# Performance work log

Hardware: AMD Instinct MI355X
Metric: run time of the kernel (lower is better)

The kernel has to match this reference:

```python
import jax, jax.numpy as jnp
import numpy as np

DIM = 4096
N_HEADS = 32
HEAD_DIM = 128
N_KV_HEADS = 8
REPEAT = N_HEADS // N_KV_HEADS  # 4
B = 8
# ragged per-sequence lengths, fixed so total token count is static (jit-friendly)
SEQLEN = np.array([1024, 3072, 2048, 2560, 1536, 2048, 1792, 2304], dtype=np.int64)
TOTAL = int(SEQLEN.sum())  # 16384


def setup_inputs() -> dict:
    key = jax.random.key(0)
    k1, k2, k3 = jax.random.split(key, 3)
    embedding = jax.random.normal(k1, (B, DIM), dtype=jnp.float32)
    # nn.Linear weights: stored as [out_features, in_features]
    W_up = jax.random.normal(k2, (N_KV_HEADS * HEAD_DIM, DIM), dtype=jnp.float32) * (DIM ** -0.5)
    W_down = jax.random.normal(k3, (DIM, N_HEADS * HEAD_DIM), dtype=jnp.float32) * ((N_HEADS * HEAD_DIM) ** -0.5)
    seqlen = jnp.asarray(SEQLEN)
    return {"embedding": embedding, "W_up": W_up, "W_down": W_down, "seqlen": seqlen}


def reference(embedding, W_up, W_down, seqlen):
    # up-projection: [B, dim] -> [B, n_kv_heads*head_dim]
    x = embedding @ W_up.T
    # split kv heads and repeat-interleave to n_heads: [B, n_kv, hd] -> [B, n_heads, hd]
    xv = x.reshape(B, N_KV_HEADS, HEAD_DIM)
    val = jnp.repeat(xv, REPEAT, axis=1).reshape(B, N_HEADS * HEAD_DIM)  # [B, dim]
    # ragged broadcast: row i repeated seqlen[i] times -> [TOTAL, dim]
    out = jnp.repeat(val, seqlen, axis=0, total_repeat_length=TOTAL)
    # down-projection on every token row (redundant per-sequence math, as in original)
    return out @ W_down.T  # [TOTAL, dim]
```

## Files before the change

### kernel.cpp

```cpp
#include <hip/hip_runtime.h>

#define DIM   4096
#define KVDIM 1024
#define NB    8
#define TOTAL 16384
#define BCAST_BLOCKS 4096

__global__ __launch_bounds__(256)
void k_up(const float* __restrict__ emb, const float* __restrict__ wup,
          float* __restrict__ x) {
    int wid  = blockIdx.x * 4 + (threadIdx.x >> 6);
    int lane = threadIdx.x & 63;
    int j = wid >> 3;
    int b = wid & 7;
    const float4* e = (const float4*)(emb + b * DIM);
    const float4* w = (const float4*)(wup + (long)j * DIM);
    float acc = 0.f;
    #pragma unroll
    for (int ii = 0; ii < DIM / 4 / 64; ii++) {
        int it = ii * 64 + lane;
        float4 ev = e[it], wv = w[it];
        acc += ev.x * wv.x + ev.y * wv.y + ev.z * wv.z + ev.w * wv.w;
    }
    #pragma unroll
    for (int off = 32; off; off >>= 1) acc += __shfl_down(acc, off, 64);
    if (lane == 0) x[b * KVDIM + j] = acc;
}

__global__ __launch_bounds__(256)
void k_down(const float* __restrict__ x, const float* __restrict__ wdn,
            float* __restrict__ y) {
    __shared__ float part[4][NB];
    int o    = blockIdx.x;
    int wv   = threadIdx.x >> 6;
    int lane = threadIdx.x & 63;
    const float4* w = (const float4*)(wdn + (long)o * DIM);
    float acc[NB];
    #pragma unroll
    for (int b = 0; b < NB; b++) acc[b] = 0.f;
    #pragma unroll
    for (int ii = 0; ii < 4; ii++) {
        int it = wv * 256 + ii * 64 + lane;
        int k0 = it * 4;
        int kv = ((k0 >> 9) << 7) + (k0 & 127);
        float4 wvv = w[it];
        #pragma unroll
        for (int b = 0; b < NB; b++) {
            const float4 xv = *(const float4*)(x + b * KVDIM + kv);
            acc[b] += xv.x * wvv.x + xv.y * wvv.y + xv.z * wvv.z + xv.w * wvv.w;
        }
    }
    #pragma unroll
    for (int b = 0; b < NB; b++) {
        #pragma unroll
        for (int off = 32; off; off >>= 1) acc[b] += __shfl_down(acc[b], off, 64);
    }
    if (lane == 0) {
        #pragma unroll
        for (int b = 0; b < NB; b++) part[wv][b] = acc[b];
    }
    __syncthreads();
    if (threadIdx.x < NB) {
        int b = threadIdx.x;
        float s = part[0][b] + part[1][b] + part[2][b] + part[3][b];
        y[b * DIM + o] = s;
    }
}

__global__ __launch_bounds__(256)
void k_bcast(const float* __restrict__ y, const int* __restrict__ seqlen,
             float4* __restrict__ out) {
    int c0 = seqlen[0];
    int c1 = c0 + seqlen[1];
    int c2 = c1 + seqlen[2];
    int c3 = c2 + seqlen[3];
    int c4 = c3 + seqlen[4];
    int c5 = c4 + seqlen[5];
    int c6 = c5 + seqlen[6];
    #pragma unroll
    for (int g = 0; g < TOTAL / BCAST_BLOCKS; g++) {
        int row = blockIdx.x + g * BCAST_BLOCKS;
        int s = (row >= c0) + (row >= c1) + (row >= c2) + (row >= c3)
              + (row >= c4) + (row >= c5) + (row >= c6);
        const float4* yr = (const float4*)(y + s * DIM);
        float4* orow = out + (long)row * (DIM / 4);
        #pragma unroll
        for (int c = threadIdx.x; c < DIM / 4; c += 256)
            orow[c] = yr[c];
    }
}

extern "C" void kernel_launch(void* const* d_in, const int* in_sizes, int n_in,
                              void* d_out, int out_size, void* d_ws, size_t ws_size,
                              hipStream_t stream) {
    const float* emb = (const float*)d_in[0];
    const float* wup = (const float*)d_in[1];
    const float* wdn = (const float*)d_in[2];
    const int* seqlen = (const int*)d_in[3];

    float* x = (float*)d_ws;
    float* y = x + NB * KVDIM;

    k_up   <<<NB * KVDIM / 4, 256, 0, stream>>>(emb, wup, x);
    k_down <<<DIM,            256, 0, stream>>>(x, wdn, y);
    k_bcast<<<BCAST_BLOCKS,   256, 0, stream>>>(y, seqlen, (float4*)d_out);
}
```

Before: 348.0 us.

## Fuse up-proj, down-proj and broadcast into one cooperative kernel with grid syncs

Replaces the three separate launches with a single cooperative kernel of 1024 blocks that runs the up-projection, a grid-wide sync, the down-projection (one wave per output column), another grid sync, and the ragged row broadcast. The aim is to remove two launch gaps and the kernel-boundary drain between stages. In exchange it uses a smaller grid for the bandwidth-bound broadcast and adds grid-barrier cost. It falls back to the old three-kernel path if the cooperative launch fails.

Measured after the change: 519.2 us. 49.2% more time.

```diff
diff --git a/kernel.cpp b/kernel.cpp
--- a/kernel.cpp
+++ b/kernel.cpp
@@ -1,10 +1,86 @@
 #include <hip/hip_runtime.h>
+#include <hip/hip_cooperative_groups.h>
+
+namespace cg = cooperative_groups;
 
 #define DIM   4096
 #define KVDIM 1024
 #define NB    8
 #define TOTAL 16384
+#define NBLK  1024
 #define BCAST_BLOCKS 4096
+
+__global__ __launch_bounds__(256, 4)
+void fused_pca(const float* __restrict__ emb, const float* __restrict__ wup,
+               const float* __restrict__ wdn, const int* __restrict__ seqlen,
+               float* __restrict__ x, float* __restrict__ y,
+               float* __restrict__ out) {
+    cg::grid_group grid = cg::this_grid();
+    const int lane = threadIdx.x & 63;
+    const int wid  = blockIdx.x * 4 + (threadIdx.x >> 6);
+
+    #pragma unroll
+    for (int i = 0; i < 2; i++) {
+        int d = wid * 2 + i;
+        int j = d >> 3;
+        int b = d & 7;
+        const float4* e = (const float4*)(emb + b * DIM);
+        const float4* w = (const float4*)(wup + (long)j * DIM);
+        float acc = 0.f;
+        for (int it = lane; it < DIM / 4; it += 64) {
+            float4 ev = e[it], wv = w[it];
+            acc += ev.x * wv.x + ev.y * wv.y + ev.z * wv.z + ev.w * wv.w;
+        }
+        #pragma unroll
+        for (int off = 32; off; off >>= 1) acc += __shfl_down(acc, off, 64);
+        if (lane == 0) x[b * KVDIM + j] = acc;
+    }
+
+    grid.sync();
+
+    {
+        int o = wid;
+        const float4* w = (const float4*)(wdn + (long)o * DIM);
+        float acc[NB];
+        #pragma unroll
+        for (int b = 0; b < NB; b++) acc[b] = 0.f;
+        for (int it = lane; it < DIM / 4; it += 64) {
+            int k0 = it * 4;
+            int kv = ((k0 >> 9) << 7) + (k0 & 127);
+            float4 wv = w[it];
+            #pragma unroll
+            for (int b = 0; b < NB; b++) {
+                const float4 xv = *(const float4*)(x + b * KVDIM + kv);
+                acc[b] += xv.x * wv.x + xv.y * wv.y + xv.z * wv.z + xv.w * wv.w;
+            }
+        }
+        #pragma unroll
+        for (int b = 0; b < NB; b++) {
+            #pragma unroll
+            for (int off = 32; off; off >>= 1) acc[b] += __shfl_down(acc[b], off, 64);
+            if (lane == 0) y[b * DIM + o] = acc[b];
+        }
+    }
+
+    grid.sync();
+
+    int c0 = seqlen[0];
+    int c1 = c0 + seqlen[1];
+    int c2 = c1 + seqlen[2];
+    int c3 = c2 + seqlen[3];
+    int c4 = c3 + seqlen[4];
+    int c5 = c4 + seqlen[5];
+    int c6 = c5 + seqlen[6];
+    for (int g = 0; g < TOTAL / NBLK; g++) {
+        int row = blockIdx.x + g * NBLK;
+        int s = (row >= c0) + (row >= c1) + (row >= c2) + (row >= c3)
+              + (row >= c4) + (row >= c5) + (row >= c6);
+        const float4* yr = (const float4*)(y + s * DIM);
+        float4* orow = (float4*)(out + (long)row * DIM);
+        for (int c = threadIdx.x; c < DIM / 4; c += 256)
+            orow[c] = yr[c];
+    }
+}
 
 __global__ __launch_bounds__(256)
 void k_up(const float* __restrict__ emb, const float* __restrict__ wup,
@@ -62,8 +138,7 @@
     __syncthreads();
     if (threadIdx.x < NB) {
         int b = threadIdx.x;
-        float s = part[0][b] + part[1][b] + part[2][b] + part[3][b];
-        y[b * DIM + o] = s;
+        y[b * DIM + o] = part[0][b] + part[1][b] + part[2][b] + part[3][b];
     }
 }
 
@@ -100,8 +175,16 @@
 
     float* x = (float*)d_ws;
     float* y = x + NB * KVDIM;
+    float* out = (float*)d_out;
 
-    k_up   <<<NB * KVDIM / 4, 256, 0, stream>>>(emb, wup, x);
-    k_down <<<DIM,            256, 0, stream>>>(x, wdn, y);
-    k_bcast<<<BCAST_BLOCKS,   256, 0, stream>>>(y, seqlen, (float4*)d_out);
+    void* args[] = {(void*)&emb, (void*)&wup, (void*)&wdn, (void*)&seqlen,
+                    (void*)&x, (void*)&y, (void*)&out};
+    hipError_t err = hipLaunchCooperativeKernel((const void*)fused_pca,
+                                                dim3(NBLK), dim3(256),
+                                                args, 0, stream);
+    if (err != hipSuccess) {
+        k_up   <<<NB * KVDIM / 4, 256, 0, stream>>>(emb, wup, x);
+        k_down <<<DIM,            256, 0, stream>>>(x, wdn, y);
+        k_bcast<<<BCAST_BLOCKS,   256, 0, stream>>>(y, seqlen, (float4*)out);
+    }
 }
```

## Fuse down-projection and broadcast with per-column-tile atomic counters

Applied to the files above, without the earlier changes.

Merges the down-projection and ragged broadcast kernels into one 1024-block kernel. Each block computes four output columns, then signals a per-64-column-tile counter. Blocks spin-wait until their tile's counter is complete and then write 64-column slabs of the output, so broadcast writes can start before the whole down-projection finishes. This removes one launch and the gap between kernels. It relies on all 64 producer blocks for a tile being co-resident or scheduled ahead, so it carries deadlock risk, and the output write pattern changes to 256-byte row segments.

Result: slower. 645.4 us (+85.5%).

```diff
diff --git a/kernel.cpp b/kernel.cpp
--- a/kernel.cpp
+++ b/kernel.cpp
@@ -4,11 +4,12 @@
 #define KVDIM 1024
 #define NB    8
 #define TOTAL 16384
-#define BCAST_BLOCKS 4096
+#define GRID2 1024
 
 __global__ __launch_bounds__(256)
 void k_up(const float* __restrict__ emb, const float* __restrict__ wup,
-          float* __restrict__ x) {
+          float* __restrict__ x, int* __restrict__ cnt) {
+    if (blockIdx.x == 0 && threadIdx.x < 16) cnt[threadIdx.x] = 0;
     int wid  = blockIdx.x * 4 + (threadIdx.x >> 6);
     int lane = threadIdx.x & 63;
     int j = wid >> 3;
@@ -17,7 +18,7 @@
     const float4* w = (const float4*)(wup + (long)j * DIM);
     float acc = 0.f;
     #pragma unroll
-    for (int ii = 0; ii < DIM / 4 / 64; ii++) {
+    for (int ii = 0; ii < 16; ii++) {
         int it = ii * 64 + lane;
         float4 ev = e[it], wv = w[it];
         acc += ev.x * wv.x + ev.y * wv.y + ev.z * wv.z + ev.w * wv.w;
@@ -28,65 +29,96 @@
 }
 
 __global__ __launch_bounds__(256)
-void k_down(const float* __restrict__ x, const float* __restrict__ wdn,
-            float* __restrict__ y) {
-    __shared__ float part[4][NB];
-    int o    = blockIdx.x;
-    int wv   = threadIdx.x >> 6;
-    int lane = threadIdx.x & 63;
-    const float4* w = (const float4*)(wdn + (long)o * DIM);
-    float acc[NB];
+void k_dc(const float* __restrict__ x, const float* __restrict__ wdn,
+          float* __restrict__ y, int* __restrict__ cnt,
+          const int* __restrict__ seqlen, float4* __restrict__ out) {
+    __shared__ float4 tile[NB][65];
+    __shared__ float  part[4][NB];
+    const int B    = blockIdx.x;
+    const int t    = threadIdx.x;
+    const int wv   = t >> 6;
+    const int lane = t & 63;
+
     #pragma unroll
-    for (int b = 0; b < NB; b++) acc[b] = 0.f;
-    #pragma unroll
-    for (int ii = 0; ii < 4; ii++) {
-        int it = wv * 256 + ii * 64 + lane;
-        int k0 = it * 4;
-        int kv = ((k0 >> 9) << 7) + (k0 & 127);
-        float4 wvv = w[it];
+    for (int i = 0; i < 4; i++) {
+        const int o = B * 4 + i;
+        const float4* w = (const float4*)(wdn + (long)o * DIM);
+        float acc[NB];
+        #pragma unroll
+        for (int b = 0; b < NB; b++) acc[b] = 0.f;
+        #pragma unroll
+        for (int ii = 0; ii < 4; ii++) {
+            int it = wv * 256 + ii * 64 + lane;
+            int k0 = it * 4;
+            int kv = ((k0 >> 9) << 7) + (k0 & 127);
+            float4 wvv = w[it];
+            #pragma unroll
+            for (int b = 0; b < NB; b++) {
+                const float4 xv = *(const float4*)(x + b * KVDIM + kv);
+                acc[b] += xv.x * wvv.x + xv.y * wvv.y + xv.z * wvv.z + xv.w * wvv.w;
+            }
+        }
         #pragma unroll
         for (int b = 0; b < NB; b++) {
-            const float4 xv = *(const float4*)(x + b * KVDIM + kv);
-            acc[b] += xv.x * wvv.x + xv.y * wvv.y + xv.z * wvv.z + xv.w * wvv.w;
+            #pragma unroll
+            for (int off = 32; off; off >>= 1) acc[b] += __shfl_down(acc[b], off, 64);
         }
+        if (lane == 0) {
+            #pragma unroll
+            for (int b = 0; b < NB; b++) part[wv][b] = acc[b];
+        }
+        __syncthreads();
+        if (t < NB)
+            y[t * DIM + o] = part[0][t] + part[1][t] + part[2][t] + part[3][t];
+        __syncthreads();
     }
-    #pragma unroll
-    for (int b = 0; b < NB; b++) {
-        #pragma unroll
-        for (int off = 32; off; off >>= 1) acc[b] += __shfl_down(acc[b], off, 64);
-    }
-    if (lane == 0) {
-        #pragma unroll
-        for (int b = 0; b < NB; b++) part[wv][b] = acc[b];
+    __threadfence();
+    __syncthreads();
+    if (t == 0)
+        __hip_atomic_fetch_add(&cnt[B >> 6], 4, __ATOMIC_RELEASE,
+                               __HIP_MEMORY_SCOPE_AGENT);
+
+    const int ct = B >> 6;
+    if (t == 0) {
+        while (__hip_atomic_load(&cnt[ct], __ATOMIC_ACQUIRE,
+                                 __HIP_MEMORY_SCOPE_AGENT) < 256)
+            __builtin_amdgcn_s_sleep(8);
     }
     __syncthreads();
-    if (threadIdx.x < NB) {
-        int b = threadIdx.x;
-        float s = part[0][b] + part[1][b] + part[2][b] + part[3][b];
-        y[b * DIM + o] = s;
-    }
-}
+    __threadfence();
 
-__global__ __launch_bounds__(256)
-void k_bcast(const float* __restrict__ y, const int* __restrict__ seqlen,
-             float4* __restrict__ out) {
-    int c0 = seqlen[0];
-    int c1 = c0 + seqlen[1];
-    int c2 = c1 + seqlen[2];
-    int c3 = c2 + seqlen[3];
-    int c4 = c3 + seqlen[4];
-    int c5 = c4 + seqlen[5];
-    int c6 = c5 + seqlen[6];
+    const int c0 = seqlen[0];
+    const int c1 = c0 + seqlen[1];
+    const int c2 = c1 + seqlen[2];
+    const int c3 = c2 + seqlen[3];
+    const int c4 = c3 + seqlen[4];
+    const int c5 = c4 + seqlen[5];
+    const int c6 = c5 + seqlen[6];
+    const float4* y4 = (const float4*)y;
+
     #pragma unroll
-    for (int g = 0; g < TOTAL / BCAST_BLOCKS; g++) {
-        int row = blockIdx.x + g * BCAST_BLOCKS;
-        int s = (row >= c0) + (row >= c1) + (row >= c2) + (row >= c3)
-              + (row >= c4) + (row >= c5) + (row >= c6);
-        const float4* yr = (const float4*)(y + s * DIM);
-        float4* orow = out + (long)row * (DIM / 4);
+    for (int i = 0; i < 4; i++) {
+        const int tl = B * 4 + i;
+        const int rt = tl & 255;
         #pragma unroll
-        for (int c = threadIdx.x; c < DIM / 4; c += 256)
-            orow[c] = yr[c];
+        for (int j = 0; j < 2; j++) {
+            int idx = j * 256 + t;
+            int s   = idx >> 6;
+            int c4i = idx & 63;
+            tile[s][c4i] = y4[s * (DIM / 4) + ct * 64 + c4i];
+        }
+        __syncthreads();
+        #pragma unroll
+        for (int j = 0; j < 16; j++) {
+            int idx = j * 256 + t;
+            int rl  = idx >> 6;
+            int c4i = idx & 63;
+            int row = rt * 64 + rl;
+            int s = (row >= c0) + (row >= c1) + (row >= c2) + (row >= c3)
+                  + (row >= c4) + (row >= c5) + (row >= c6);
+            out[(long)row * (DIM / 4) + ct * 64 + c4i] = tile[s][c4i];
+        }
+        __syncthreads();
     }
 }
 
@@ -98,10 +130,11 @@
     const float* wdn = (const float*)d_in[2];
     const int* seqlen = (const int*)d_in[3];
 
-    float* x = (float*)d_ws;
-    float* y = x + NB * KVDIM;
+    float* x   = (float*)d_ws;
+    float* y   = x + NB * KVDIM;
+    int*   cnt = (int*)(y + NB * DIM);
 
-    k_up   <<<NB * KVDIM / 4, 256, 0, stream>>>(emb, wup, x);
-    k_down <<<DIM,            256, 0, stream>>>(x, wdn, y);
-    k_bcast<<<BCAST_BLOCKS,   256, 0, stream>>>(y, seqlen, (float4*)d_out);
+    k_up<<<NB * KVDIM / 4, 256, 0, stream>>>(emb, wup, x, cnt);
+    k_dc<<<GRID2,          256, 0, stream>>>(x, wdn, y, cnt, seqlen,
+                                             (float4*)d_out);
 }
```
